# Kernel optimization log

Measured on AMD Instinct MI355X. Metric: run time of the kernel, lower is better.

Reference implementation:

```python
import jax, jax.numpy as jnp
import numpy as np

B, C, H, W = 8, 256, 128, 128
EPS = 1e-12  # F.normalize eps


def setup_inputs() -> dict:
    key = jax.random.key(0)
    k0, k1, k2, k3 = jax.random.split(key, 4)
    x = jax.random.normal(k0, (B, C, H, W), jnp.float32)
    # qkv: Conv2d(C, 3C, 1, bias=False) -> weight [3C, C]
    w_qkv = jax.random.normal(k1, (3 * C, C), jnp.float32) * 0.02
    # qkv_dwconv: Conv2d(3C, 3C, 1, groups=3C) -> per-channel scale [3C]
    w_dw = jax.random.normal(k2, (3 * C,), jnp.float32) * 0.1 + 1.0
    # temperature: Parameter(ones(num_heads=1, 1, 1))
    temperature = jnp.ones((1, 1, 1), jnp.float32)
    # project_out: Conv2d(C, C, 1, bias=False) -> weight [C, C]
    w_proj = jax.random.normal(k3, (C, C), jnp.float32) * 0.02
    return {"x": x, "w_qkv": w_qkv, "w_dw": w_dw,
            "temperature": temperature, "w_proj": w_proj}


def reference(x, w_qkv, w_dw, temperature, w_proj):
    b, c, h, w = x.shape
    n = h * w
    # pointwise conv + depthwise 1x1 conv (= per-channel scale)
    qkv = jnp.einsum('bchw,oc->bohw', x, w_qkv) * w_dw[None, :, None, None]
    q, k, v = jnp.split(qkv, 3, axis=1)          # each [b, c, h, w]
    q = q.reshape(b, c, n)
    k = k.reshape(b, c, n)
    v = v.reshape(b, c, n)
    # L2-normalize along spatial dim (F.normalize: x / max(||x||, eps))
    q = q / jnp.maximum(jnp.linalg.norm(q, axis=-1, keepdims=True), EPS)
    k = k / jnp.maximum(jnp.linalg.norm(k, axis=-1, keepdims=True), EPS)
    # channel-wise cosine attention: [b, c, c]
    attn = jnp.einsum('bcn,bdn->bcd', q, k) * temperature[0]
    attn = jax.nn.softmax(attn, axis=-1)
    out = jnp.einsum('bcd,bdn->bcn', attn, v).reshape(b, c, h, w)
    out = jnp.einsum('bchw,oc->bohw', out, w_proj)
    return out
```

## Files before the change

kernel.cpp:

```cpp
#include <hip/hip_runtime.h>
#include <hip/hip_bf16.h>
#include <stdint.h>

#define NB 8
#define NC 256
#define NN 16384
#define KS 32

typedef short bf16x8 __attribute__((ext_vector_type(8)));
typedef float f32x4  __attribute__((ext_vector_type(4)));
typedef uint32_t u32;

__device__ __forceinline__ unsigned short f2bf(float f) {
  union { float f; unsigned u; } c; c.f = f;
  return (unsigned short)((c.u + 0x7FFFu + ((c.u >> 16) & 1u)) >> 16);
}

__device__ __forceinline__ bf16x8 pack8(float4 lo, float4 hi) {
  union { bf16x8 v; __hip_bfloat162 h[4]; } u;
  u.h[0] = __float22bfloat162_rn(make_float2(lo.x, lo.y));
  u.h[1] = __float22bfloat162_rn(make_float2(lo.z, lo.w));
  u.h[2] = __float22bfloat162_rn(make_float2(hi.x, hi.y));
  u.h[3] = __float22bfloat162_rn(make_float2(hi.z, hi.w));
  return u.v;
}

__device__ __forceinline__ void gload16(const void* g, void* l) {
  __builtin_amdgcn_global_load_lds(
      (const __attribute__((address_space(1))) u32*)g,
      (__attribute__((address_space(3))) u32*)l, 16, 0, 0);
}

__device__ __forceinline__ void stage_tile(const char* src, int ld_bytes,
                                           char* lds, int w, int l) {
#pragma unroll
  for (int i = 0; i < 4; ++i) {
    int s = (w * 4 + i) * 64 + l;
    int row = s >> 3;
    int srcslot = (l & 7) ^ (row & 7);
    gload16(src + (size_t)row * ld_bytes + srcslot * 16,
            lds + (w * 4 + i) * 1024);
  }
}

__device__ __forceinline__ void gemm_core(const char* A, int lda_b,
                                          const char* Bm, int ldb_b, int ktiles,
                                          char* smem, int tid, f32x4 acc[4][4]) {
  const int w = tid >> 6, l = tid & 63;
  const int wm = w >> 1, wn = w & 1;
  char* As = smem;
  char* Bs = smem + 16384;
  for (int kt = 0; kt < ktiles; ++kt) {
    stage_tile(A + kt * 128, lda_b, As, w, l);
    stage_tile(Bm + kt * 128, ldb_b, Bs, w, l);
    __syncthreads();
#pragma unroll
    for (int ks = 0; ks < 2; ++ks) {
      bf16x8 av[4], bv[4];
      const int kb = ks * 64 + ((l >> 4) << 4);
#pragma unroll
      for (int m = 0; m < 4; ++m) {
        int row = wm * 64 + m * 16 + (l & 15);
        av[m] = *(const bf16x8*)(As + row * 128 + (kb ^ ((row & 7) << 4)));
      }
#pragma unroll
      for (int nq = 0; nq < 4; ++nq) {
        int row = wn * 64 + nq * 16 + (l & 15);
        bv[nq] = *(const bf16x8*)(Bs + row * 128 + (kb ^ ((row & 7) << 4)));
      }
#pragma unroll
      for (int m = 0; m < 4; ++m)
#pragma unroll
        for (int nq = 0; nq < 4; ++nq)
          acc[m][nq] = __builtin_amdgcn_mfma_f32_16x16x32_bf16(
              av[m], bv[nq], acc[m][nq], 0, 0, 0);
    }
    __syncthreads();
  }
}

__global__ __launch_bounds__(256) void k_prepw2(const float* __restrict__ wqkv,
                                                const float* __restrict__ wdw,
                                                float* __restrict__ Wcat,
                                                float* __restrict__ WkT,
                                                float* __restrict__ Wv2) {
  const int r = blockIdx.x, t = threadIdx.x;
  Wcat[r * 256 + t] = wqkv[r * 256 + t] * wdw[r];
  float kv = wqkv[(256 + r) * 256 + t] * wdw[256 + r];
  Wcat[65536 + r * 256 + t] = kv;
  WkT[t * 256 + r] = kv;
  Wv2[r * 256 + t] = wqkv[(512 + r) * 256 + t] * wdw[512 + r];
}

__global__ __launch_bounds__(512, 2) void k_gramT(const float* __restrict__ x,
                                                  float* __restrict__ gpart,
                                                  char* __restrict__ xt) {
  __shared__ __align__(16) float tile[256 * 64];
  const int tid = threadIdx.x;
  const int ks = blockIdx.x, b = blockIdx.y;
  const int w = tid >> 6, l = tid & 63;
  const int wm = w >> 2, wn = w & 3;
  f32x4 acc[8][4];
#pragma unroll
  for (int m = 0; m < 8; ++m)
#pragma unroll
    for (int n = 0; n < 4; ++n) acc[m][n] = (f32x4){0.f, 0.f, 0.f, 0.f};
  const float* x0 = x + (size_t)b * NC * NN + (size_t)ks * 512;

  for (int kt = 0; kt < 8; ++kt) {
#pragma unroll
    for (int i = 0; i < 8; ++i) {
      int c = (w * 8 + i) * 64 + l;
      int row = c >> 4, slot = c & 15;
      int sl = slot ^ (row & 15);
      gload16(x0 + (size_t)row * NN + kt * 64 + sl * 4,
              (char*)tile + (w * 8 + i) * 1024);
    }
    __syncthreads();
#pragma unroll
    for (int ks2 = 0; ks2 < 2; ++ks2) {
      const int s0 = ks2 * 8 + (l >> 4) * 2;
      bf16x8 av[8], bv[4];
#pragma unroll
      for (int m = 0; m < 8; ++m) {
        int row = wm * 128 + m * 16 + (l & 15);
        float4 lo = *(const float4*)&tile[row * 64 + ((s0 ^ (row & 15)) * 4)];
        float4 hi = *(const float4*)&tile[row * 64 + (((s0 + 1) ^ (row & 15)) * 4)];
        av[m] = pack8(lo, hi);
      }
#pragma unroll
      for (int n = 0; n < 4; ++n) {
        int row = wn * 64 + n * 16 + (l & 15);
        float4 lo = *(const float4*)&tile[row * 64 + ((s0 ^ (row & 15)) * 4)];
        float4 hi = *(const float4*)&tile[row * 64 + (((s0 + 1) ^ (row & 15)) * 4)];
        bv[n] = pack8(lo, hi);
      }
#pragma unroll
      for (int m = 0; m < 8; ++m)
#pragma unroll
        for (int n = 0; n < 4; ++n)
          acc[m][n] = __builtin_amdgcn_mfma_f32_16x16x32_bf16(
              av[m], bv[n], acc[m][n], 0, 0, 0);
    }
    {
      const int n4 = tid >> 5, c8 = tid & 31;
      const int gn = ks * 512 + kt * 64 + n4 * 4;
      float vr[8][4];
#pragma unroll
      for (int j = 0; j < 8; ++j) {
        int c = c8 * 8 + j;
        float4 v = *(const float4*)&tile[c * 64 + ((n4 ^ (c & 15)) * 4)];
        vr[j][0] = v.x; vr[j][1] = v.y; vr[j][2] = v.z; vr[j][3] = v.w;
      }
#pragma unroll
      for (int k = 0; k < 4; ++k) {
        unsigned short ov[8] __attribute__((aligned(16)));
#pragma unroll
        for (int j = 0; j < 8; ++j) ov[j] = f2bf(vr[j][k]);
        *(uint4*)(xt + (((size_t)b * NN + gn + k) * 256 + c8 * 8) * 2) =
            *(const uint4*)(ov);
      }
    }
    __syncthreads();
  }
  float* gp = gpart + ((size_t)(ks * NB + b)) * 65536;
#pragma unroll
  for (int m = 0; m < 8; ++m)
#pragma unroll
    for (int n = 0; n < 4; ++n)
#pragma unroll
      for (int r = 0; r < 4; ++r) {
        int c = wm * 128 + m * 16 + ((l >> 4) << 2) + r;
        int d = wn * 64 + n * 16 + (l & 15);
        gp[(size_t)c * 256 + d] = acc[m][n][r];
      }
}

__global__ __launch_bounds__(256) void k_reduceG(const float* __restrict__ gpart,
                                                 float* __restrict__ G) {
  const int t = threadIdx.x, c = blockIdx.x, b = blockIdx.y;
  float s = 0.f;
#pragma unroll
  for (int ks = 0; ks < KS; ++ks)
    s += gpart[(((size_t)ks * NB + b) * 256 + c) * 256 + t];
  G[((size_t)b * 256 + c) * 256 + t] = s;
}

__global__ __launch_bounds__(256) void k_sgT(const float* __restrict__ Wcat,
                                             const float* __restrict__ G,
                                             float* __restrict__ T12,
                                             float* __restrict__ nqk) {
  const int t = threadIdx.x;
  const int r0 = blockIdx.x * 8, b = blockIdx.y;
  const float* Gb = G + (size_t)b * 65536 + t;
  float acc[8] = {0, 0, 0, 0, 0, 0, 0, 0};
#pragma unroll 4
  for (int k = 0; k < 256; ++k) {
    float bv = Gb[(size_t)k * 256];
#pragma unroll
    for (int o = 0; o < 8; ++o) acc[o] += Wcat[(r0 + o) * 256 + k] * bv;
  }
#pragma unroll
  for (int o = 0; o < 8; ++o)
    T12[(size_t)b * 131072 + (size_t)(r0 + o) * 256 + t] = acc[o];
  __shared__ float red[8][4];
  const int w = t >> 6, l = t & 63;
#pragma unroll
  for (int o = 0; o < 8; ++o) {
    float s = acc[o] * Wcat[(r0 + o) * 256 + t];
#pragma unroll
    for (int off = 32; off; off >>= 1) s += __shfl_xor(s, off);
    if (l == 0) red[o][w] = s;
  }
  __syncthreads();
  if (t < 8)
    nqk[b * 512 + r0 + t] = red[t][0] + red[t][1] + red[t][2] + red[t][3];
}

__global__ __launch_bounds__(256) void k_ssoft(const float* __restrict__ T12,
                                               const float* __restrict__ WkT,
                                               const float* __restrict__ nqk,
                                               const float* __restrict__ temp,
                                               float* __restrict__ attn) {
  const int t = threadIdx.x;
  const int c0 = blockIdx.x * 8, b = blockIdx.y;
  const float* Ab = T12 + (size_t)b * 131072 + (size_t)c0 * 256;
  const float* Bb = WkT + t;
  float acc[8] = {0, 0, 0, 0, 0, 0, 0, 0};
#pragma unroll 4
  for (int k = 0; k < 256; ++k) {
    float bv = Bb[(size_t)k * 256];
#pragma unroll
    for (int o = 0; o < 8; ++o) acc[o] += Ab[o * 256 + k] * bv;
  }
  const float rk = 1.0f / fmaxf(sqrtf(fmaxf(nqk[b * 512 + 256 + t], 0.f)), 1e-12f);
  const float tau = temp[0];
#pragma unroll
  for (int o = 0; o < 8; ++o) {
    float rq = 1.0f / fmaxf(sqrtf(fmaxf(nqk[b * 512 + c0 + o], 0.f)), 1e-12f);
    acc[o] = acc[o] * rq * rk * tau;
  }
  __shared__ float redm[8][4];
  __shared__ float reds[8][4];
  const int w = t >> 6, l = t & 63;
#pragma unroll
  for (int o = 0; o < 8; ++o) {
    float m = acc[o];
#pragma unroll
    for (int off = 32; off; off >>= 1) m = fmaxf(m, __shfl_xor(m, off));
    if (l == 0) redm[o][w] = m;
  }
  __syncthreads();
  float e[8];
#pragma unroll
  for (int o = 0; o < 8; ++o) {
    float m = fmaxf(fmaxf(redm[o][0], redm[o][1]), fmaxf(redm[o][2], redm[o][3]));
    e[o] = __expf(acc[o] - m);
    float s = e[o];
#pragma unroll
    for (int off = 32; off; off >>= 1) s += __shfl_xor(s, off);
    if (l == 0) reds[o][w] = s;
  }
  __syncthreads();
#pragma unroll
  for (int o = 0; o < 8; ++o) {
    float tot = reds[o][0] + reds[o][1] + reds[o][2] + reds[o][3];
    attn[(size_t)b * 65536 + (size_t)(c0 + o) * 256 + t] = e[o] / tot;
  }
}

__global__ __launch_bounds__(256) void k_sg2x(const float* __restrict__ wp,
                                              const float* __restrict__ attn,
                                              const float* __restrict__ wv2,
                                              char* __restrict__ Fb) {
  __shared__ float P[8 * 256];
  const int t = threadIdx.x;
  const int o0 = blockIdx.x * 8, b = blockIdx.y;
  const float* Ab = wp + (size_t)o0 * 256;
  const float* Bb = attn + (size_t)b * 65536 + t;
  float acc[8] = {0, 0, 0, 0, 0, 0, 0, 0};
#pragma unroll 4
  for (int k = 0; k < 256; ++k) {
    float bv = Bb[(size_t)k * 256];
#pragma unroll
    for (int o = 0; o < 8; ++o) acc[o] += Ab[o * 256 + k] * bv;
  }
#pragma unroll
  for (int o = 0; o < 8; ++o) P[o * 256 + t] = acc[o];
  __syncthreads();
  float a2[8] = {0, 0, 0, 0, 0, 0, 0, 0};
  const float* Bv = wv2 + t;
#pragma unroll 4
  for (int k = 0; k < 256; ++k) {
    float bv = Bv[(size_t)k * 256];
#pragma unroll
    for (int o = 0; o < 8; ++o) a2[o] += P[o * 256 + k] * bv;
  }
  unsigned short* Cp = (unsigned short*)Fb + (size_t)b * 65536;
#pragma unroll
  for (int o = 0; o < 8; ++o) Cp[(size_t)(o0 + o) * 256 + t] = f2bf(a2[o]);
}

__global__ __launch_bounds__(256) void k_final(const char* __restrict__ xt,
                                               const char* __restrict__ fb,
                                               float* __restrict__ out) {
  __shared__ char smem[65536];
  const int tid = threadIdx.x;
  const int nt = blockIdx.x, ot = blockIdx.y, b = blockIdx.z;
  f32x4 acc[4][4];
#pragma unroll
  for (int m = 0; m < 4; ++m)
#pragma unroll
    for (int nq = 0; nq < 4; ++nq) acc[m][nq] = (f32x4){0.f, 0.f, 0.f, 0.f};
  const char* Ap = xt + ((size_t)b * NN + (size_t)nt * 128) * 512;
  const char* Bp = fb + ((size_t)(b * 256 + ot * 128)) * 512;
  gemm_core(Ap, 512, Bp, 512, 4, smem, tid, acc);
  const int w = tid >> 6, l = tid & 63, wm = w >> 1, wn = w & 1;
#pragma unroll
  for (int m = 0; m < 4; ++m)
#pragma unroll
    for (int nq = 0; nq < 4; ++nq)
#pragma unroll
      for (int r = 0; r < 4; ++r) {
        int i = wm * 64 + m * 16 + ((l >> 4) << 2) + r;
        int j = wn * 64 + nq * 16 + (l & 15);
        *(float*)(smem + j * 512 + ((i * 4) ^ ((j & 7) << 4))) = acc[m][nq][r];
      }
  __syncthreads();
  const int j = tid >> 1, h = tid & 1;
  float* dst = out + ((size_t)(b * 256 + ot * 128 + j)) * NN + nt * 128;
#pragma unroll
  for (int cc = 0; cc < 16; ++cc) {
    int ch = h * 16 + cc;
    *(uint4*)(dst + ch * 4) =
        *(const uint4*)(smem + j * 512 + ((ch * 16) ^ ((j & 7) << 4)));
  }
}

extern "C" void kernel_launch(void* const* d_in, const int* in_sizes, int n_in,
                              void* d_out, int out_size, void* d_ws, size_t ws_size,
                              hipStream_t stream) {
  const float* x     = (const float*)d_in[0];
  const float* wqkv  = (const float*)d_in[1];
  const float* wdwf  = (const float*)d_in[2];
  const float* temp  = (const float*)d_in[3];
  const float* wproj = (const float*)d_in[4];
  float* out = (float*)d_out;
  char* ws = (char*)d_ws;

  char*  xt    = ws;
  float* gpart = (float*)(ws + 67108864);
  float* G     = (float*)(ws + 134217728);
  float* T12   = (float*)(ws + 136314880);
  float* attn  = (float*)(ws + 140509184);
  char*  Fb    = ws + 142606336;
  float* Wcat  = (float*)(ws + 143654912);
  float* WkT   = (float*)(ws + 144179200);
  float* Wv2   = (float*)(ws + 144441344);
  float* nqk   = (float*)(ws + 144703488);

  k_prepw2<<<dim3(256), dim3(256), 0, stream>>>(wqkv, wdwf, Wcat, WkT, Wv2);
  k_gramT<<<dim3(KS, NB), dim3(512), 0, stream>>>(x, gpart, xt);
  k_reduceG<<<dim3(256, NB), dim3(256), 0, stream>>>(gpart, G);
  k_sgT<<<dim3(64, NB), dim3(256), 0, stream>>>(Wcat, G, T12, nqk);
  k_ssoft<<<dim3(32, NB), dim3(256), 0, stream>>>(T12, WkT, nqk, temp, attn);
  k_sg2x<<<dim3(32, NB), dim3(256), 0, stream>>>(wproj, attn, Wv2, Fb);
  k_final<<<dim3(128, 2, NB), dim3(256), 0, stream>>>(xt, Fb, out);
}
```

Before: 253.7 us.

## Split Gram kernel across two row tiles and halve final-kernel LDS staging

The Gram kernel grid is doubled with a new row-tile dimension. Each block computes half of the 256x256 output rows, with half the accumulators, and writes half of the transposed bf16 copy of x. Both blocks still load the full 256x512 input slice, so global reads of x double in exchange for more blocks and lower register pressure on the 256-CU device. The final GEMM epilogue now stages its output through LDS in two 64-column passes using 32KB instead of 64KB, which is meant to allow more resident blocks.

```diff
diff --git a/kernel.cpp b/kernel.cpp
--- a/kernel.cpp
+++ b/kernel.cpp
@@ -97,12 +97,12 @@
                                                   char* __restrict__ xt) {
   __shared__ __align__(16) float tile[256 * 64];
   const int tid = threadIdx.x;
-  const int ks = blockIdx.x, b = blockIdx.y;
+  const int mt = blockIdx.x, ks = blockIdx.y, b = blockIdx.z;
   const int w = tid >> 6, l = tid & 63;
-  const int wm = w >> 2, wn = w & 3;
-  f32x4 acc[8][4];
-#pragma unroll
-  for (int m = 0; m < 8; ++m)
+  const int wm = (w >> 2) & 1, wn = w & 3;
+  f32x4 acc[4][4];
+#pragma unroll
+  for (int m = 0; m < 4; ++m)
 #pragma unroll
     for (int n = 0; n < 4; ++n) acc[m][n] = (f32x4){0.f, 0.f, 0.f, 0.f};
   const float* x0 = x + (size_t)b * NC * NN + (size_t)ks * 512;
@@ -120,10 +120,10 @@
 #pragma unroll
     for (int ks2 = 0; ks2 < 2; ++ks2) {
       const int s0 = ks2 * 8 + (l >> 4) * 2;
-      bf16x8 av[8], bv[4];
-#pragma unroll
-      for (int m = 0; m < 8; ++m) {
-        int row = wm * 128 + m * 16 + (l & 15);
+      bf16x8 av[4], bv[4];
+#pragma unroll
+      for (int m = 0; m < 4; ++m) {
+        int row = mt * 128 + wm * 64 + m * 16 + (l & 15);
         float4 lo = *(const float4*)&tile[row * 64 + ((s0 ^ (row & 15)) * 4)];
         float4 hi = *(const float4*)&tile[row * 64 + (((s0 + 1) ^ (row & 15)) * 4)];
         av[m] = pack8(lo, hi);
@@ -136,14 +136,16 @@
         bv[n] = pack8(lo, hi);
       }
 #pragma unroll
-      for (int m = 0; m < 8; ++m)
+      for (int m = 0; m < 4; ++m)
 #pragma unroll
         for (int n = 0; n < 4; ++n)
           acc[m][n] = __builtin_amdgcn_mfma_f32_16x16x32_bf16(
               av[m], bv[n], acc[m][n], 0, 0, 0);
     }
     {
-      const int n4 = tid >> 5, c8 = tid & 31;
+      const int half = tid >> 8;
+      const int n4 = (tid >> 4) & 15;
+      const int c8 = mt * 16 + (tid & 15);
       const int gn = ks * 512 + kt * 64 + n4 * 4;
       float vr[8][4];
 #pragma unroll
@@ -153,7 +155,8 @@
         vr[j][0] = v.x; vr[j][1] = v.y; vr[j][2] = v.z; vr[j][3] = v.w;
       }
 #pragma unroll
-      for (int k = 0; k < 4; ++k) {
+      for (int kk = 0; kk < 2; ++kk) {
+        const int k = half * 2 + kk;
         unsigned short ov[8] __attribute__((aligned(16)));
 #pragma unroll
         for (int j = 0; j < 8; ++j) ov[j] = f2bf(vr[j][k]);
@@ -165,12 +168,12 @@
   }
   float* gp = gpart + ((size_t)(ks * NB + b)) * 65536;
 #pragma unroll
-  for (int m = 0; m < 8; ++m)
+  for (int m = 0; m < 4; ++m)
 #pragma unroll
     for (int n = 0; n < 4; ++n)
 #pragma unroll
       for (int r = 0; r < 4; ++r) {
-        int c = wm * 128 + m * 16 + ((l >> 4) << 2) + r;
+        int c = mt * 128 + wm * 64 + m * 16 + ((l >> 4) << 2) + r;
         int d = wn * 64 + n * 16 + (l & 15);
         gp[(size_t)c * 256 + d] = acc[m][n][r];
       }
@@ -304,7 +307,7 @@
 __global__ __launch_bounds__(256) void k_final(const char* __restrict__ xt,
                                                const char* __restrict__ fb,
                                                float* __restrict__ out) {
-  __shared__ char smem[65536];
+  __shared__ char smem[32768];
   const int tid = threadIdx.x;
   const int nt = blockIdx.x, ot = blockIdx.y, b = blockIdx.z;
   f32x4 acc[4][4];
@@ -315,25 +318,31 @@
   const char* Ap = xt + ((size_t)b * NN + (size_t)nt * 128) * 512;
   const char* Bp = fb + ((size_t)(b * 256 + ot * 128)) * 512;
   gemm_core(Ap, 512, Bp, 512, 4, smem, tid, acc);
-  const int w = tid >> 6, l = tid & 63, wm = w >> 1, wn = w & 1;
-#pragma unroll
-  for (int m = 0; m < 4; ++m)
-#pragma unroll
-    for (int nq = 0; nq < 4; ++nq)
-#pragma unroll
-      for (int r = 0; r < 4; ++r) {
-        int i = wm * 64 + m * 16 + ((l >> 4) << 2) + r;
-        int j = wn * 64 + nq * 16 + (l & 15);
-        *(float*)(smem + j * 512 + ((i * 4) ^ ((j & 7) << 4))) = acc[m][nq][r];
-      }
-  __syncthreads();
-  const int j = tid >> 1, h = tid & 1;
-  float* dst = out + ((size_t)(b * 256 + ot * 128 + j)) * NN + nt * 128;
-#pragma unroll
-  for (int cc = 0; cc < 16; ++cc) {
-    int ch = h * 16 + cc;
-    *(uint4*)(dst + ch * 4) =
-        *(const uint4*)(smem + j * 512 + ((ch * 16) ^ ((j & 7) << 4)));
+  const int w = tid >> 6, l = tid & 63, wn = w & 1, wm = w >> 1;
+#pragma unroll
+  for (int p = 0; p < 2; ++p) {
+    __syncthreads();
+    if (wn == p) {
+#pragma unroll
+      for (int m = 0; m < 4; ++m)
+#pragma unroll
+        for (int nq = 0; nq < 4; ++nq)
+#pragma unroll
+          for (int r = 0; r < 4; ++r) {
+            int i = wm * 64 + m * 16 + ((l >> 4) << 2) + r;
+            int j = nq * 16 + (l & 15);
+            *(float*)(smem + j * 512 + ((i * 4) ^ ((j & 7) << 4))) = acc[m][nq][r];
+          }
+    }
+    __syncthreads();
+    const int jj = tid >> 2, h = tid & 3;
+    float* dst = out + ((size_t)(b * 256 + ot * 128 + p * 64 + jj)) * NN + nt * 128;
+#pragma unroll
+    for (int cc = 0; cc < 8; ++cc) {
+      int ch = h * 8 + cc;
+      *(uint4*)(dst + ch * 4) =
+          *(const uint4*)(smem + jj * 512 + ((ch * 16) ^ ((jj & 7) << 4)));
+    }
   }
 }
 
@@ -360,7 +369,7 @@
   float* nqk   = (float*)(ws + 144703488);
 
   k_prepw2<<<dim3(256), dim3(256), 0, stream>>>(wqkv, wdwf, Wcat, WkT, Wv2);
-  k_gramT<<<dim3(KS, NB), dim3(512), 0, stream>>>(x, gpart, xt);
+  k_gramT<<<dim3(2, KS, NB), dim3(512), 0, stream>>>(x, gpart, xt);
   k_reduceG<<<dim3(256, NB), dim3(256), 0, stream>>>(gpart, G);
   k_sgT<<<dim3(64, NB), dim3(256), 0, stream>>>(Wcat, G, T12, nqk);
   k_ssoft<<<dim3(32, NB), dim3(256), 0, stream>>>(T12, WkT, nqk, temp, attn);
```

After: 310.9 us. 22.5% more time.

## Double split-K partitions for Gram kernel and store partials as bf16

Applied to the files above, without the earlier changes.

The Gram-matrix kernel now splits the spatial dimension into 64 chunks instead of 32, giving 512 blocks, and its launch bound is raised to ask for 4 blocks per SM. Partial Gram tiles are written as bf16 instead of fp32, so the partial buffer stays the same size despite twice as many partials. The reduction kernel reads packed bf16 pairs and sums them in fp32. The aim is better GPU occupancy and less partial-sum traffic, at the cost of rounding the partials to bf16, which loses precision in the Gram matrix that feeds the softmax. The higher launch bound may also pressure registers with the 128-float accumulator.

```diff
diff --git a/kernel.cpp b/kernel.cpp
--- a/kernel.cpp
+++ b/kernel.cpp
@@ -5,7 +5,7 @@
 #define NB 8
 #define NC 256
 #define NN 16384
-#define KS 32
+#define KS 64
 
 typedef short bf16x8 __attribute__((ext_vector_type(8)));
 typedef float f32x4  __attribute__((ext_vector_type(4)));
@@ -14,6 +14,10 @@
 __device__ __forceinline__ unsigned short f2bf(float f) {
   union { float f; unsigned u; } c; c.f = f;
   return (unsigned short)((c.u + 0x7FFFu + ((c.u >> 16) & 1u)) >> 16);
+}
+__device__ __forceinline__ float bf2f(unsigned short h) {
+  union { unsigned u; float f; } c; c.u = ((unsigned)h) << 16;
+  return c.f;
 }
 
 __device__ __forceinline__ bf16x8 pack8(float4 lo, float4 hi) {
@@ -92,8 +96,8 @@
   Wv2[r * 256 + t] = wqkv[(512 + r) * 256 + t] * wdw[512 + r];
 }
 
-__global__ __launch_bounds__(512, 2) void k_gramT(const float* __restrict__ x,
-                                                  float* __restrict__ gpart,
+__global__ __launch_bounds__(512, 4) void k_gramT(const float* __restrict__ x,
+                                                  unsigned short* __restrict__ gpart,
                                                   char* __restrict__ xt) {
   __shared__ __align__(16) float tile[256 * 64];
   const int tid = threadIdx.x;
@@ -105,9 +109,9 @@
   for (int m = 0; m < 8; ++m)
 #pragma unroll
     for (int n = 0; n < 4; ++n) acc[m][n] = (f32x4){0.f, 0.f, 0.f, 0.f};
-  const float* x0 = x + (size_t)b * NC * NN + (size_t)ks * 512;
-
-  for (int kt = 0; kt < 8; ++kt) {
+  const float* x0 = x + (size_t)b * NC * NN + (size_t)ks * 256;
+
+  for (int kt = 0; kt < 4; ++kt) {
 #pragma unroll
     for (int i = 0; i < 8; ++i) {
       int c = (w * 8 + i) * 64 + l;
@@ -144,7 +148,7 @@
     }
     {
       const int n4 = tid >> 5, c8 = tid & 31;
-      const int gn = ks * 512 + kt * 64 + n4 * 4;
+      const int gn = ks * 256 + kt * 64 + n4 * 4;
       float vr[8][4];
 #pragma unroll
       for (int j = 0; j < 8; ++j) {
@@ -163,7 +167,7 @@
     }
     __syncthreads();
   }
-  float* gp = gpart + ((size_t)(ks * NB + b)) * 65536;
+  unsigned short* gp = gpart + ((size_t)(ks * NB + b)) * 65536;
 #pragma unroll
   for (int m = 0; m < 8; ++m)
 #pragma unroll
@@ -172,18 +176,23 @@
       for (int r = 0; r < 4; ++r) {
         int c = wm * 128 + m * 16 + ((l >> 4) << 2) + r;
         int d = wn * 64 + n * 16 + (l & 15);
-        gp[(size_t)c * 256 + d] = acc[m][n][r];
-      }
-}
-
-__global__ __launch_bounds__(256) void k_reduceG(const float* __restrict__ gpart,
-                                                 float* __restrict__ G) {
-  const int t = threadIdx.x, c = blockIdx.x, b = blockIdx.y;
-  float s = 0.f;
-#pragma unroll
-  for (int ks = 0; ks < KS; ++ks)
-    s += gpart[(((size_t)ks * NB + b) * 256 + c) * 256 + t];
-  G[((size_t)b * 256 + c) * 256 + t] = s;
+        gp[(size_t)c * 256 + d] = f2bf(acc[m][n][r]);
+      }
+}
+
+__global__ __launch_bounds__(256) void k_reduceG(
+    const unsigned short* __restrict__ gpart, float* __restrict__ G) {
+  const int t = threadIdx.x;
+  const int c = blockIdx.x * 2 + (t >> 7), b = blockIdx.y;
+  const int d0 = (t & 127) * 2;
+  float s0 = 0.f, s1 = 0.f;
+#pragma unroll 8
+  for (int ks = 0; ks < KS; ++ks) {
+    u32 v = *(const u32*)(gpart + (((size_t)ks * NB + b) * 256 + c) * 256 + d0);
+    s0 += bf2f((unsigned short)(v & 0xffff));
+    s1 += bf2f((unsigned short)(v >> 16));
+  }
+  *(float2*)(G + ((size_t)b * 256 + c) * 256 + d0) = make_float2(s0, s1);
 }
 
 __global__ __launch_bounds__(256) void k_sgT(const float* __restrict__ Wcat,
@@ -349,7 +358,7 @@
   char* ws = (char*)d_ws;
 
   char*  xt    = ws;
-  float* gpart = (float*)(ws + 67108864);
+  unsigned short* gpart = (unsigned short*)(ws + 67108864);
   float* G     = (float*)(ws + 134217728);
   float* T12   = (float*)(ws + 136314880);
   float* attn  = (float*)(ws + 140509184);
@@ -361,7 +370,7 @@
 
   k_prepw2<<<dim3(256), dim3(256), 0, stream>>>(wqkv, wdwf, Wcat, WkT, Wv2);
   k_gramT<<<dim3(KS, NB), dim3(512), 0, stream>>>(x, gpart, xt);
-  k_reduceG<<<dim3(256, NB), dim3(256), 0, stream>>>(gpart, G);
+  k_reduceG<<<dim3(128, NB), dim3(256), 0, stream>>>(gpart, G);
   k_sgT<<<dim3(64, NB), dim3(256), 0, stream>>>(Wcat, G, T12, nqk);
   k_ssoft<<<dim3(32, NB), dim3(256), 0, stream>>>(T12, WkT, nqk, temp, attn);
   k_sg2x<<<dim3(32, NB), dim3(256), 0, stream>>>(wproj, attn, Wv2, Fb);
```

Result: slower. 431.6 us (+70.1%).
